# Optimization experiments

Hardware: AMD Instinct MI355X
Metric: run time of the kernel (lower is better)

The kernel has to match this reference:

```python
import jax, jax.numpy as jnp
import numpy as np
from jax import lax

B, H, S = 256, 256, 512


def setup_inputs() -> dict:
    key = jax.random.key(0)
    ks = jax.random.split(key, 7)
    sc = 1.0 / np.sqrt(H).astype(np.float32)
    tree_state = jax.random.normal(ks[0], (B, H), jnp.float32)
    seq_states = jax.random.normal(ks[1], (B, H, S), jnp.float32)
    seq_mask = jax.random.randint(ks[2], (B, S), 0, 2, jnp.int32)
    W_ih = jax.random.uniform(ks[3], (3 * H, H), jnp.float32, -sc, sc)
    W_hh = jax.random.uniform(ks[4], (3 * H, H), jnp.float32, -sc, sc)
    b_ih = jax.random.uniform(ks[5], (3 * H,), jnp.float32, -sc, sc)
    b_hh = jax.random.uniform(ks[6], (3 * H,), jnp.float32, -sc, sc)
    return {"tree_state": tree_state, "seq_states": seq_states, "seq_mask": seq_mask,
            "W_ih": W_ih, "W_hh": W_hh, "b_ih": b_ih, "b_hh": b_hh}


def _gru_cell(x, h, W_ih, W_hh, b_ih, b_hh):
    # torch.nn.GRUCell math. x, h: (B, H); W_*: (3H, H); b_*: (3H,)
    gi = x @ W_ih.T + b_ih          # (B, 3H)
    gh = h @ W_hh.T + b_hh          # (B, 3H)
    i_r, i_z, i_n = jnp.split(gi, 3, axis=-1)
    h_r, h_z, h_n = jnp.split(gh, 3, axis=-1)
    r = jax.nn.sigmoid(i_r + h_r)
    z = jax.nn.sigmoid(i_z + h_z)
    n = jnp.tanh(i_n + r * h_n)
    return (1.0 - z) * n + z * h


def reference(tree_state, seq_states, seq_mask, W_ih, W_hh, b_ih, b_hh):
    # sequential recurrent scan over the seq axis of seq_states (batch, hid, seq)
    xs = jnp.transpose(seq_states, (2, 0, 1))  # (S, B, H)

    def step(h, x):
        h_new = _gru_cell(x, h, W_ih, W_hh, b_ih, b_hh)
        return h_new, h_new

    _, outs = lax.scan(step, tree_state, xs)      # (S, B, H)
    rnn_out = jnp.transpose(outs, (1, 0, 2))      # (B, S, H)
    # get_final_encoder_states: last unmasked timestep per row
    last_idx = jnp.maximum(jnp.sum(seq_mask, axis=1) - 1, 0)  # (B,)
    final = jnp.take_along_axis(rnn_out, last_idx[:, None, None], axis=1)  # (B,1,H)
    return final[:, 0, :]
```

## Files before the change

kernel.cpp:

```cpp
#include <hip/hip_runtime.h>
#include <hip/hip_bf16.h>

#define HH 256
#define SSL 512
#define G3 768

using short8 = __attribute__((ext_vector_type(8))) short;
using f32x4  = __attribute__((ext_vector_type(4))) float;

__device__ __forceinline__ unsigned short f2bf(float f) {
  unsigned int u = __float_as_uint(f);
  u += 0x7FFFu + ((u >> 16) & 1u);
  return (unsigned short)(u >> 16);
}
__device__ __forceinline__ float bf2f(unsigned short b) {
  return __uint_as_float(((unsigned int)b) << 16);
}
__device__ __forceinline__ void sync_step() {
  asm volatile("s_waitcnt lgkmcnt(0)" ::: "memory");
  __builtin_amdgcn_s_barrier();
  __builtin_amdgcn_sched_barrier(0);
}

__global__ __launch_bounds__(256) void prep_pack(
    const float* __restrict__ Wih, const float* __restrict__ Whh,
    unsigned short* __restrict__ wih_bf, unsigned short* __restrict__ whh_frag)
{
  int blk = blockIdx.x;
  if (blk < 96) {
    int base = (blk * 256 + threadIdx.x) * 4;
#pragma unroll
    for (int i = 0; i < 4; i++) {
      int u = base + i;
      float a = Wih[2 * u], b = Wih[2 * u + 1];
      ((unsigned int*)wih_bf)[u] = (unsigned int)f2bf(a) | ((unsigned int)f2bf(b) << 16);
    }
  } else {
    int gid = (blk - 96) * 256 + threadIdx.x;
    int f = gid >> 6, l = gid & 63;
    int kt = f & 7, mt = (f >> 3) & 3, g = (f >> 5) % 3, w = f / 96;
    int row = g * HH + w * 64 + mt * 16 + (l & 15);
    int k0  = kt * 32 + (l >> 4) * 8;
    const float* src = Whh + (size_t)row * HH + k0;
    unsigned int o[4];
#pragma unroll
    for (int i = 0; i < 4; i++)
      o[i] = (unsigned int)f2bf(src[2 * i]) | ((unsigned int)f2bf(src[2 * i + 1]) << 16);
    *(uint4*)(whh_frag + ((size_t)f * 64 + l) * 8) = *(uint4*)o;
  }
}

__global__ __launch_bounds__(512, 4) void gi_gemm(
    const float* __restrict__ X, const unsigned short* __restrict__ Wb,
    const float* __restrict__ bih, const float* __restrict__ bhh,
    unsigned short* __restrict__ gi)
{
  __shared__ __align__(16) char smem[36864];
  unsigned short* Al = (unsigned short*)smem;
  unsigned short* Bl = (unsigned short*)(smem + 16384);
  float (*Dl)[132] = (float(*)[132])smem;

  const int tid  = threadIdx.x;
  const int lane = tid & 63;
  const int wave = tid >> 6;
  const int wm   = wave >> 2;
  const int wj   = wave & 3;
  const int n16  = lane & 15;
  const int quad = lane >> 4;

  const int mblk = blockIdx.y;
  const int b    = mblk >> 2;
  const int s0   = (mblk & 3) * 128;
  const int j0   = blockIdx.x * 128;

  f32x4 acc[4][2];
#pragma unroll
  for (int mt = 0; mt < 4; mt++)
#pragma unroll
    for (int jt = 0; jt < 2; jt++) acc[mt][jt] = f32x4{0.f, 0.f, 0.f, 0.f};

  const float* Xb = X + (size_t)b * (HH * SSL);

  float4 xa[2][2];
  uint4  wbv[2];

  auto ldA = [&](int kt, int q, float4* dst) {
    int idx = tid + 512 * q, sq = idx & 31, a = idx >> 5;
    const float* p = Xb + (size_t)(kt * 64 + 2 * a) * SSL + s0 + 4 * sq;
    dst[0] = *(const float4*)p;
    dst[1] = *(const float4*)(p + SSL);
  };
  auto ldB = [&](int kt, int q) -> uint4 {
    int cid = tid + 512 * q, j = cid >> 3, c = cid & 7;
    return *(const uint4*)(Wb + (size_t)(j0 + j) * HH + kt * 64 + c * 8);
  };

  ldA(0, 0, xa[0]); ldA(0, 1, xa[1]);
  wbv[0] = ldB(0, 0); wbv[1] = ldB(0, 1);

  for (int kt = 0; kt < 4; kt++) {
#pragma unroll
    for (int q = 0; q < 2; q++) {
      int idx = tid + 512 * q, sq = idx & 31, a = idx >> 5;
      int c = a >> 2, d = a & 3;
#pragma unroll
      for (int r = 0; r < 4; r++) {
        int s = 4 * sq + r;
        int sw = (s + (s >> 3)) & 7;
        unsigned int u =
            (unsigned int)f2bf(((const float*)&xa[q][0])[r]) |
            ((unsigned int)f2bf(((const float*)&xa[q][1])[r]) << 16);
        *(unsigned int*)(Al + s * 64 + ((c ^ sw) * 8) + d * 2) = u;
      }
    }
#pragma unroll
    for (int p = 0; p < 2; p++) {
      int cid = tid + 512 * p, j = cid >> 3, c = cid & 7;
      int sw = (j + (j >> 3)) & 7;
      *(uint4*)(Bl + j * 64 + ((c ^ sw) * 8)) = wbv[p];
    }
    __syncthreads();
    if (kt < 3) {
      ldA(kt + 1, 0, xa[0]); ldA(kt + 1, 1, xa[1]);
      wbv[0] = ldB(kt + 1, 0); wbv[1] = ldB(kt + 1, 1);
    }
#pragma unroll
    for (int kk = 0; kk < 2; kk++) {
      short8 af[4], bfr[2];
#pragma unroll
      for (int mt = 0; mt < 4; mt++) {
        int s = wm * 64 + mt * 16 + n16;
        int sw = (s + (s >> 3)) & 7;
        af[mt] = *(const short8*)(Al + s * 64 + (((kk * 4 + quad) ^ sw) * 8));
      }
#pragma unroll
      for (int jt = 0; jt < 2; jt++) {
        int j = wj * 32 + jt * 16 + n16;
        int sw = (j + (j >> 3)) & 7;
        bfr[jt] = *(const short8*)(Bl + j * 64 + (((kk * 4 + quad) ^ sw) * 8));
      }
#pragma unroll
      for (int mt = 0; mt < 4; mt++)
#pragma unroll
        for (int jt = 0; jt < 2; jt++)
          acc[mt][jt] = __builtin_amdgcn_mfma_f32_16x16x32_bf16(af[mt], bfr[jt], acc[mt][jt], 0, 0, 0);
    }
    __syncthreads();
  }

  float bias[2];
  {
    int jg0 = j0 + wj * 32 + 0 * 16 + n16;
    int jg1 = j0 + wj * 32 + 1 * 16 + n16;
    bias[0] = bih[jg0] + (jg0 < 2 * HH ? bhh[jg0] : 0.f);
    bias[1] = bih[jg1] + (jg1 < 2 * HH ? bhh[jg1] : 0.f);
  }

  for (int c = 0; c < 2; c++) {
    __syncthreads();
    if (wm == c) {
#pragma unroll
      for (int mt = 0; mt < 4; mt++)
#pragma unroll
        for (int jt = 0; jt < 2; jt++)
#pragma unroll
          for (int r = 0; r < 4; r++)
            Dl[mt * 16 + quad * 4 + r][wj * 32 + jt * 16 + n16] = acc[mt][jt][r] + bias[jt];
    }
    __syncthreads();
#pragma unroll
    for (int i = 0; i < 2; i++) {
      int ml = (tid >> 4) + 32 * i;
      int jj = (tid & 15) * 8;
      float4 p0 = *(const float4*)&Dl[ml][jj];
      float4 p1 = *(const float4*)&Dl[ml][jj + 4];
      short8 st;
      st[0] = (short)f2bf(p0.x); st[1] = (short)f2bf(p0.y);
      st[2] = (short)f2bf(p0.z); st[3] = (short)f2bf(p0.w);
      st[4] = (short)f2bf(p1.x); st[5] = (short)f2bf(p1.y);
      st[6] = (short)f2bf(p1.z); st[7] = (short)f2bf(p1.w);
      int sgl = s0 + c * 64 + ml;
      *(short8*)(gi + ((size_t)b * SSL + sgl) * G3 + j0 + jj) = st;
    }
  }
}

__global__ __launch_bounds__(256, 1) void gru_scan(
    const float* __restrict__ tree, const int* __restrict__ mask,
    const unsigned short* __restrict__ wfrag, const float* __restrict__ bhh,
    const unsigned short* __restrict__ gi, float* __restrict__ out)
{
  __shared__ __align__(16) unsigned short hbuf[2][1088];
  __shared__ int lsum[4];

  const int tid  = threadIdx.x;
  const int lane = tid & 63;
  const int w    = tid >> 6;
  const int n16  = lane & 15;
  const int quad = lane >> 4;
  const int b    = n16 & 3;
  const int rep  = n16 >> 2;
  const int brow0 = blockIdx.x * 4;
  const int jbase = w * 64 + rep * 16 + quad * 4;

  if (tid < 4) lsum[tid] = 0;

  f32x4 h4 = *(const f32x4*)(tree + (size_t)(brow0 + b) * HH + jbase);

  const int wslot = ((w * 2 + (rep >> 1)) * 17 + b * 4 + ((rep & 1) * 2 + (quad >> 1))) * 8
                  + (quad & 1) * 4;
  {
    unsigned long long u =
        (unsigned long long)((unsigned)f2bf(h4[0]) | ((unsigned)f2bf(h4[1]) << 16)) |
        ((unsigned long long)((unsigned)f2bf(h4[2]) | ((unsigned)f2bf(h4[3]) << 16)) << 32);
    *(unsigned long long*)&hbuf[0][wslot] = u;
  }
  {
    const int* mp = mask + (size_t)(brow0 + w) * SSL + lane * 8;
    int4 a = *(const int4*)mp;
    int4 c = *(const int4*)(mp + 4);
    atomicAdd(&lsum[w], a.x + a.y + a.z + a.w + c.x + c.y + c.z + c.w);
  }

  short8 awA[2][4][8];
  short8 awV[4][8];
#pragma unroll
  for (int g = 0; g < 2; g++)
#pragma unroll
    for (int mt = 0; mt < 4; mt++)
#pragma unroll
      for (int kt = 0; kt < 8; kt++) {
        int F = ((w * 3 + g) * 4 + mt) * 8 + kt;
        awA[g][mt][kt] = *(const short8*)(wfrag + ((size_t)F * 64 + lane) * 8);
      }
#pragma unroll
  for (int mt = 0; mt < 4; mt++)
#pragma unroll
    for (int kt = 0; kt < 8; kt++) {
      int F = ((w * 3 + 2) * 4 + mt) * 8 + kt;
      awV[mt][kt] = *(const short8*)(wfrag + ((size_t)F * 64 + lane) * 8);
    }
#pragma unroll
  for (int g = 0; g < 2; g++)
#pragma unroll
    for (int mt = 0; mt < 4; mt++)
#pragma unroll
      for (int kt = 0; kt < 8; kt++)
        asm volatile("" : "+a"(awA[g][mt][kt]));
#pragma unroll
  for (int mt = 0; mt < 4; mt++)
#pragma unroll
    for (int kt = 0; kt < 8; kt++)
      asm volatile("" : "+v"(awV[mt][kt]));

  f32x4 bh4 = *(const f32x4*)(bhh + 2 * HH + jbase);

  const unsigned short* gip = gi + (size_t)(brow0 + b) * SSL * G3 + jbase;
  unsigned long long gA[3], gB[3];
#pragma unroll
  for (int g = 0; g < 3; g++) gA[g] = *(const unsigned long long*)(gip + (size_t)0 * G3 + g * HH);
#pragma unroll
  for (int g = 0; g < 3; g++) gB[g] = *(const unsigned long long*)(gip + (size_t)1 * G3 + g * HH);

  __syncthreads();
  int mylast = lsum[b] - 1; if (mylast < 0) mylast = 0;

  auto step = [&](int t, unsigned long long* gv) {
    const int cb = t & 1, nb = cb ^ 1;
    unsigned long long g0 = gv[0], g1 = gv[1], g2 = gv[2];

    const unsigned short* hp = &hbuf[cb][0] + ((n16 & 3) * 4 + quad) * 8;
    short8 hb[8];
#pragma unroll
    for (int kt = 0; kt < 8; kt++)
      hb[kt] = *(const short8*)(hp + kt * (17 * 8));

    int tn = (t + 2 < SSL) ? t + 2 : SSL - 1;
    gv[0] = *(const unsigned long long*)(gip + (size_t)tn * G3 + 0 * HH);
    gv[1] = *(const unsigned long long*)(gip + (size_t)tn * G3 + 1 * HH);
    gv[2] = *(const unsigned long long*)(gip + (size_t)tn * G3 + 2 * HH);

    f32x4 selR, selZ, selN;
#pragma unroll
    for (int mp = 0; mp < 2; mp++) {
      const int m0 = 2 * mp, m1 = 2 * mp + 1;
      f32x4 ar0 = f32x4{0.f, 0.f, 0.f, 0.f}, az0 = ar0, an0 = ar0;
      f32x4 ar1 = ar0, az1 = ar0, an1 = ar0;
#pragma unroll
      for (int kt = 0; kt < 8; kt++) {
        ar0 = __builtin_amdgcn_mfma_f32_16x16x32_bf16(awA[0][m0][kt], hb[kt], ar0, 0, 0, 0);
        ar1 = __builtin_amdgcn_mfma_f32_16x16x32_bf16(awA[0][m1][kt], hb[kt], ar1, 0, 0, 0);
        az0 = __builtin_amdgcn_mfma_f32_16x16x32_bf16(awA[1][m0][kt], hb[kt], az0, 0, 0, 0);
        az1 = __builtin_amdgcn_mfma_f32_16x16x32_bf16(awA[1][m1][kt], hb[kt], az1, 0, 0, 0);
        an0 = __builtin_amdgcn_mfma_f32_16x16x32_bf16(awV[m0][kt],    hb[kt], an0, 0, 0, 0);
        an1 = __builtin_amdgcn_mfma_f32_16x16x32_bf16(awV[m1][kt],    hb[kt], an1, 0, 0, 0);
      }
      if (mp == 0) {
        selR = (rep == 0) ? ar0 : ar1;
        selZ = (rep == 0) ? az0 : az1;
        selN = (rep == 0) ? an0 : an1;
      } else {
        selR = (rep == 2) ? ar0 : ((rep == 3) ? ar1 : selR);
        selZ = (rep == 2) ? az0 : ((rep == 3) ? az1 : selZ);
        selN = (rep == 2) ? an0 : ((rep == 3) ? an1 : selN);
      }
    }

#pragma unroll
    for (int e = 0; e < 4; e++) {
      float gr = bf2f((unsigned short)((g0 >> (16 * e)) & 0xFFFFull));
      float gz = bf2f((unsigned short)((g1 >> (16 * e)) & 0xFFFFull));
      float gn = bf2f((unsigned short)((g2 >> (16 * e)) & 0xFFFFull));
      float r = __builtin_amdgcn_rcpf(1.f + __expf(-(selR[e] + gr)));
      float z = __builtin_amdgcn_rcpf(1.f + __expf(-(selZ[e] + gz)));
      float a = gn + r * (selN[e] + bh4[e]);
      float nn = 1.f - 2.f * __builtin_amdgcn_rcpf(__expf(2.f * a) + 1.f);
      h4[e] = nn + z * (h4[e] - nn);
    }
    {
      unsigned long long u =
          (unsigned long long)((unsigned)f2bf(h4[0]) | ((unsigned)f2bf(h4[1]) << 16)) |
          ((unsigned long long)((unsigned)f2bf(h4[2]) | ((unsigned)f2bf(h4[3]) << 16)) << 32);
      *(unsigned long long*)&hbuf[nb][wslot] = u;
    }
    if (t == mylast) {
      *(f32x4*)(out + (size_t)(brow0 + b) * HH + jbase) = h4;
    }
    sync_step();
  };

  for (int t = 0; t < SSL; t += 2) {
    step(t, gA);
    step(t + 1, gB);
  }
}

extern "C" void kernel_launch(void* const* d_in, const int* in_sizes, int n_in,
                              void* d_out, int out_size, void* d_ws, size_t ws_size,
                              hipStream_t stream) {
  const float* tree = (const float*)d_in[0];
  const float* seq  = (const float*)d_in[1];
  const int*   mask = (const int*)d_in[2];
  const float* Wih  = (const float*)d_in[3];
  const float* Whh  = (const float*)d_in[4];
  const float* bih  = (const float*)d_in[5];
  const float* bhh  = (const float*)d_in[6];
  float* out = (float*)d_out;

  unsigned short* gi      = (unsigned short*)d_ws;
  unsigned short* wih_bf  = (unsigned short*)((char*)d_ws + 201326592);
  unsigned short* whh_frag= (unsigned short*)((char*)d_ws + 201719808);

  prep_pack<<<192, 256, 0, stream>>>(Wih, Whh, wih_bf, whh_frag);
  gi_gemm<<<dim3(6, 1024), 512, 0, stream>>>(seq, wih_bf, bih, bhh, gi);
  gru_scan<<<64, 256, 0, stream>>>(tree, mask, whh_frag, bhh, gi, out);
}
```

Before: 912.5 us.

## Keep full-K X tile resident in LDS and loop over all gate column blocks

Restructures the input-projection GEMM so each block loads its whole 128x256 slice of the fp32 sequence input once, converts it to bf16 in LDS, and keeps its A fragments in registers while looping over all six 128-wide column blocks of W_ih. Before, the grid was split over column blocks, so the large fp32 input was re-read and re-converted six times. The epilogue now stages bf16 instead of fp32 and takes the bias from LDS. In exchange LDS use grows to roughly 150KB, occupancy drops (launch bounds 4 to 2), and the weight loads between column blocks are not overlapped with compute.

```diff
diff --git a/kernel.cpp b/kernel.cpp
--- a/kernel.cpp
+++ b/kernel.cpp
@@ -50,55 +50,45 @@
   }
 }
 
-__global__ __launch_bounds__(512, 4) void gi_gemm(
+__global__ __launch_bounds__(512, 2) void gi_gemm(
     const float* __restrict__ X, const unsigned short* __restrict__ Wb,
     const float* __restrict__ bih, const float* __restrict__ bhh,
     unsigned short* __restrict__ gi)
 {
-  __shared__ __align__(16) char smem[36864];
-  unsigned short* Al = (unsigned short*)smem;
-  unsigned short* Bl = (unsigned short*)(smem + 16384);
-  float (*Dl)[132] = (float(*)[132])smem;
+  __shared__ __align__(16) unsigned short Al[128 * 256];
+  __shared__ __align__(16) unsigned short Bl[128 * 256];
+  __shared__ __align__(16) unsigned short Dl[64][136];
+  __shared__ float biasl[G3];
 
   const int tid  = threadIdx.x;
   const int lane = tid & 63;
   const int wave = tid >> 6;
   const int wm   = wave >> 2;
-  const int wj   = wave & 3;
+  const int wn   = wave & 3;
   const int n16  = lane & 15;
   const int quad = lane >> 4;
 
-  const int mblk = blockIdx.y;
+  const int mblk = blockIdx.x;
   const int b    = mblk >> 2;
   const int s0   = (mblk & 3) * 128;
-  const int j0   = blockIdx.x * 128;
-
-  f32x4 acc[4][2];
-#pragma unroll
-  for (int mt = 0; mt < 4; mt++)
-#pragma unroll
-    for (int jt = 0; jt < 2; jt++) acc[mt][jt] = f32x4{0.f, 0.f, 0.f, 0.f};
 
   const float* Xb = X + (size_t)b * (HH * SSL);
 
-  float4 xa[2][2];
-  uint4  wbv[2];
-
-  auto ldA = [&](int kt, int q, float4* dst) {
-    int idx = tid + 512 * q, sq = idx & 31, a = idx >> 5;
-    const float* p = Xb + (size_t)(kt * 64 + 2 * a) * SSL + s0 + 4 * sq;
-    dst[0] = *(const float4*)p;
-    dst[1] = *(const float4*)(p + SSL);
-  };
-  auto ldB = [&](int kt, int q) -> uint4 {
-    int cid = tid + 512 * q, j = cid >> 3, c = cid & 7;
-    return *(const uint4*)(Wb + (size_t)(j0 + j) * HH + kt * 64 + c * 8);
-  };
-
-  ldA(0, 0, xa[0]); ldA(0, 1, xa[1]);
-  wbv[0] = ldB(0, 0); wbv[1] = ldB(0, 1);
-
-  for (int kt = 0; kt < 4; kt++) {
+  for (int i = tid; i < G3; i += 512)
+    biasl[i] = bih[i] + (i < 2 * HH ? bhh[i] : 0.f);
+
+  float4 xs[4][2][2];
+#pragma unroll
+  for (int kt = 0; kt < 4; kt++)
+#pragma unroll
+    for (int q = 0; q < 2; q++) {
+      int idx = tid + 512 * q, sq = idx & 31, a = idx >> 5;
+      const float* p = Xb + (size_t)(kt * 64 + 2 * a) * SSL + s0 + 4 * sq;
+      xs[kt][q][0] = *(const float4*)p;
+      xs[kt][q][1] = *(const float4*)(p + SSL);
+    }
+#pragma unroll
+  for (int kt = 0; kt < 4; kt++)
 #pragma unroll
     for (int q = 0; q < 2; q++) {
       int idx = tid + 512 * q, sq = idx & 31, a = idx >> 5;
@@ -108,79 +98,108 @@
         int s = 4 * sq + r;
         int sw = (s + (s >> 3)) & 7;
         unsigned int u =
-            (unsigned int)f2bf(((const float*)&xa[q][0])[r]) |
-            ((unsigned int)f2bf(((const float*)&xa[q][1])[r]) << 16);
-        *(unsigned int*)(Al + s * 64 + ((c ^ sw) * 8) + d * 2) = u;
-      }
-    }
-#pragma unroll
-    for (int p = 0; p < 2; p++) {
-      int cid = tid + 512 * p, j = cid >> 3, c = cid & 7;
+            (unsigned int)f2bf(((const float*)&xs[kt][q][0])[r]) |
+            ((unsigned int)f2bf(((const float*)&xs[kt][q][1])[r]) << 16);
+        *(unsigned int*)(Al + s * 256 + kt * 64 + ((c ^ sw) * 8) + d * 2) = u;
+      }
+    }
+
+  {
+    uint4 wv[8];
+#pragma unroll
+    for (int p = 0; p < 8; p++) {
+      int cid = tid + 512 * p, j = cid >> 5, c = cid & 31;
+      wv[p] = *(const uint4*)(Wb + (size_t)(0 * 128 + j) * HH + c * 8);
+    }
+#pragma unroll
+    for (int p = 0; p < 8; p++) {
+      int cid = tid + 512 * p, j = cid >> 5, c = cid & 31;
       int sw = (j + (j >> 3)) & 7;
-      *(uint4*)(Bl + j * 64 + ((c ^ sw) * 8)) = wbv[p];
+      *(uint4*)(Bl + j * 256 + (c >> 3) * 64 + (((c & 7) ^ sw) * 8)) = wv[p];
+    }
+  }
+  __syncthreads();
+
+  short8 af[4][8];
+#pragma unroll
+  for (int mt = 0; mt < 4; mt++) {
+    int s = wm * 64 + mt * 16 + n16;
+    int sw = (s + (s >> 3)) & 7;
+#pragma unroll
+    for (int kkk = 0; kkk < 8; kkk++) {
+      int kt = kkk >> 1, c3 = (kkk & 1) * 4 + quad;
+      af[mt][kkk] = *(const short8*)(Al + s * 256 + kt * 64 + ((c3 ^ sw) * 8));
+    }
+  }
+
+  for (int jb = 0; jb < 6; jb++) {
+    float bb0 = biasl[jb * 128 + wn * 32 + 0 * 16 + n16];
+    float bb1 = biasl[jb * 128 + wn * 32 + 1 * 16 + n16];
+
+    f32x4 acc[4][2];
+#pragma unroll
+    for (int mt = 0; mt < 4; mt++)
+#pragma unroll
+      for (int nt = 0; nt < 2; nt++) acc[mt][nt] = f32x4{0.f, 0.f, 0.f, 0.f};
+
+#pragma unroll
+    for (int kkk = 0; kkk < 8; kkk++) {
+      short8 bfr[2];
+      int kt = kkk >> 1, c3 = (kkk & 1) * 4 + quad;
+#pragma unroll
+      for (int nt = 0; nt < 2; nt++) {
+        int j = wn * 32 + nt * 16 + n16;
+        int sw = (j + (j >> 3)) & 7;
+        bfr[nt] = *(const short8*)(Bl + j * 256 + kt * 64 + ((c3 ^ sw) * 8));
+      }
+#pragma unroll
+      for (int mt = 0; mt < 4; mt++)
+#pragma unroll
+        for (int nt = 0; nt < 2; nt++)
+          acc[mt][nt] = __builtin_amdgcn_mfma_f32_16x16x32_bf16(af[mt][kkk], bfr[nt], acc[mt][nt], 0, 0, 0);
     }
     __syncthreads();
-    if (kt < 3) {
-      ldA(kt + 1, 0, xa[0]); ldA(kt + 1, 1, xa[1]);
-      wbv[0] = ldB(kt + 1, 0); wbv[1] = ldB(kt + 1, 1);
-    }
-#pragma unroll
-    for (int kk = 0; kk < 2; kk++) {
-      short8 af[4], bfr[2];
-#pragma unroll
-      for (int mt = 0; mt < 4; mt++) {
-        int s = wm * 64 + mt * 16 + n16;
-        int sw = (s + (s >> 3)) & 7;
-        af[mt] = *(const short8*)(Al + s * 64 + (((kk * 4 + quad) ^ sw) * 8));
-      }
-#pragma unroll
-      for (int jt = 0; jt < 2; jt++) {
-        int j = wj * 32 + jt * 16 + n16;
+
+#pragma unroll
+    for (int c = 0; c < 2; c++) {
+      if (wm == c) {
+#pragma unroll
+        for (int mt = 0; mt < 4; mt++)
+#pragma unroll
+          for (int nt = 0; nt < 2; nt++) {
+            float bb = nt ? bb1 : bb0;
+#pragma unroll
+            for (int r = 0; r < 4; r++)
+              Dl[mt * 16 + quad * 4 + r][wn * 32 + nt * 16 + n16] =
+                  f2bf(acc[mt][nt][r] + bb);
+          }
+      }
+      __syncthreads();
+      {
+        int row = tid >> 3, seg = tid & 7;
+        short8 v0 = *(const short8*)&Dl[row][seg * 16];
+        short8 v1 = *(const short8*)&Dl[row][seg * 16 + 8];
+        size_t go = ((size_t)(b * SSL + s0 + c * 64 + row)) * G3 + jb * 128 + seg * 16;
+        *(short8*)(gi + go) = v0;
+        *(short8*)(gi + go + 8) = v1;
+      }
+      __syncthreads();
+    }
+
+    if (jb < 5) {
+      uint4 wv[8];
+#pragma unroll
+      for (int p = 0; p < 8; p++) {
+        int cid = tid + 512 * p, j = cid >> 5, c = cid & 31;
+        wv[p] = *(const uint4*)(Wb + (size_t)((jb + 1) * 128 + j) * HH + c * 8);
+      }
+#pragma unroll
+      for (int p = 0; p < 8; p++) {
+        int cid = tid + 512 * p, j = cid >> 5, c = cid & 31;
         int sw = (j + (j >> 3)) & 7;
-        bfr[jt] = *(const short8*)(Bl + j * 64 + (((kk * 4 + quad) ^ sw) * 8));
-      }
-#pragma unroll
-      for (int mt = 0; mt < 4; mt++)
-#pragma unroll
-        for (int jt = 0; jt < 2; jt++)
-          acc[mt][jt] = __builtin_amdgcn_mfma_f32_16x16x32_bf16(af[mt], bfr[jt], acc[mt][jt], 0, 0, 0);
-    }
-    __syncthreads();
-  }
-
-  float bias[2];
-  {
-    int jg0 = j0 + wj * 32 + 0 * 16 + n16;
-    int jg1 = j0 + wj * 32 + 1 * 16 + n16;
-    bias[0] = bih[jg0] + (jg0 < 2 * HH ? bhh[jg0] : 0.f);
-    bias[1] = bih[jg1] + (jg1 < 2 * HH ? bhh[jg1] : 0.f);
-  }
-
-  for (int c = 0; c < 2; c++) {
-    __syncthreads();
-    if (wm == c) {
-#pragma unroll
-      for (int mt = 0; mt < 4; mt++)
-#pragma unroll
-        for (int jt = 0; jt < 2; jt++)
-#pragma unroll
-          for (int r = 0; r < 4; r++)
-            Dl[mt * 16 + quad * 4 + r][wj * 32 + jt * 16 + n16] = acc[mt][jt][r] + bias[jt];
-    }
-    __syncthreads();
-#pragma unroll
-    for (int i = 0; i < 2; i++) {
-      int ml = (tid >> 4) + 32 * i;
-      int jj = (tid & 15) * 8;
-      float4 p0 = *(const float4*)&Dl[ml][jj];
-      float4 p1 = *(const float4*)&Dl[ml][jj + 4];
-      short8 st;
-      st[0] = (short)f2bf(p0.x); st[1] = (short)f2bf(p0.y);
-      st[2] = (short)f2bf(p0.z); st[3] = (short)f2bf(p0.w);
-      st[4] = (short)f2bf(p1.x); st[5] = (short)f2bf(p1.y);
-      st[6] = (short)f2bf(p1.z); st[7] = (short)f2bf(p1.w);
-      int sgl = s0 + c * 64 + ml;
-      *(short8*)(gi + ((size_t)b * SSL + sgl) * G3 + j0 + jj) = st;
+        *(uint4*)(Bl + j * 256 + (c >> 3) * 64 + (((c & 7) ^ sw) * 8)) = wv[p];
+      }
+      __syncthreads();
     }
   }
 }
@@ -352,6 +371,6 @@
   unsigned short* whh_frag= (unsigned short*)((char*)d_ws + 201719808);
 
   prep_pack<<<192, 256, 0, stream>>>(Wih, Whh, wih_bf, whh_frag);
-  gi_gemm<<<dim3(6, 1024), 512, 0, stream>>>(seq, wih_bf, bih, bhh, gi);
+  gi_gemm<<<1024, 512, 0, stream>>>(seq, wih_bf, bih, bhh, gi);
   gru_scan<<<64, 256, 0, stream>>>(tree, mask, whh_frag, bhh, gi, out);
 }
```

Result: faster. 874.2 us (-4.2%).
